# Optimization experiments

Hardware: AMD Instinct MI355X
Metric: run time of the kernel (lower is better)

The kernel has to match this reference:

```python
import jax, jax.numpy as jnp
import numpy as np

VOXEL_SIZE = 0.05  # init kwarg


def setup_inputs() -> dict:
    key = jax.random.key(0)
    N, B = 4_194_304, 16
    # coords uniform in [0, 5)^3 -> ~100^3 voxel cells per scene at voxel_size=0.05
    coord = jax.random.uniform(key, (N, 3), dtype=jnp.float32) * 5.0
    # cumulative batch offsets (equal-sized scenes), as pointops expects
    offset = (jnp.arange(1, B + 1, dtype=jnp.int32) * (N // B)).astype(jnp.int32)
    return {"coord": coord, "offset": offset}


def _voxel_mean(coord, offset, voxel_size):
    """Faithful jax port of voxelize_helper + segment_csr(mean) + batch2offset.

    Returns:
      n_p    [N,3]  voxel-mean coords, padded with zeros beyond n_voxels
      n_o    [B]    cumulative voxel counts per batch (batch2offset)
      counts [N]    points per voxel (idx_ptr = concat([0], cumsum(counts[valid])))
    """
    N = coord.shape[0]
    B = offset.shape[0]
    # batch id per point from cumulative offsets
    batch = jnp.searchsorted(offset, jnp.arange(N), side='right')  # [N]
    # start = per-batch min coord (start=None path of voxelize_helper)
    start = jax.ops.segment_min(coord, batch, num_segments=B)      # [B,3]
    grid = jnp.floor((coord - start[batch]) / voxel_size).astype(jnp.int32)  # [N,3]
    G = jnp.max(grid) + 1  # grid extent (per-axis upper bound)
    # linearized cluster key: unique per (batch, gx, gy, gz)
    ckey = ((batch * G + grid[:, 0]) * G + grid[:, 1]) * G + grid[:, 2]
    fill = B * G * G * G  # sentinel beyond any real key
    # sorted unique cluster keys == CSR segment order after sorting cluster indices
    uniq, inv = jnp.unique(ckey, return_inverse=True, size=N, fill_value=fill)
    # fused gather + segment-mean (equivalent to coord[sorted_idx] -> segment_csr mean)
    seg_sum = jax.ops.segment_sum(coord, inv, num_segments=N)                 # [N,3]
    counts = jax.ops.segment_sum(jnp.ones((N,), coord.dtype), inv, num_segments=N)
    n_p = seg_sum / jnp.maximum(counts, 1.0)[:, None]
    # batch id per voxel -> batch2offset (cumulative voxel counts)
    valid = uniq < fill
    vbatch = jnp.where(valid, uniq // (G * G * G), B)
    per_batch = jax.ops.segment_sum(valid.astype(jnp.int32), vbatch, num_segments=B + 1)[:B]
    n_o = jnp.cumsum(per_batch)
    return n_p, n_o, counts.astype(jnp.int32)


def reference(coord, offset):
    return _voxel_mean(coord, offset, VOXEL_SIZE)
```

## Files before the change

### kernel.cpp

```cpp
#include <hip/hip_runtime.h>
#include <stdint.h>


typedef unsigned int uint;
typedef unsigned long long u64;

#define VS 0.05f
#define QSCALE (4096.0f / VS)
#define QINV  (VS / 4096.0f)
#define NBUCKET 2048
#define CPB 16384
#define NBLK_P 256
#define DENSE_MAX 8192

__device__ __forceinline__ uint f2m(float f) {
    uint b = __float_as_uint(f);
    return (b & 0x80000000u) ? ~b : (b | 0x80000000u);
}
__device__ __forceinline__ float m2f(uint m) {
    uint b = (m & 0x80000000u) ? (m & 0x7fffffffu) : ~m;
    return __uint_as_float(b);
}

__global__ void k_init(uint* start_m, int B3) {
    int i = blockIdx.x * blockDim.x + threadIdx.x;
    if (i < B3) start_m[i] = 0xFFFFFFFFu;
}

__global__ void k_minmax(const float* __restrict__ coord, const int* __restrict__ offset,
                         int N, int B, uint* start_m) {
    __shared__ uint smin[768];
    __shared__ int soff[256];
    int nb3 = B * 3;
    for (int j = threadIdx.x; j < B; j += blockDim.x) soff[j] = offset[j];
    for (int j = threadIdx.x; j < nb3; j += blockDim.x) smin[j] = 0xFFFFFFFFu;
    __syncthreads();
    int lane = threadIdx.x & 63;
    int stride = gridDim.x * blockDim.x;
    for (int i = blockIdx.x * blockDim.x + threadIdx.x; i < N; i += stride) {
        float x = coord[3 * i + 0], y = coord[3 * i + 1], z = coord[3 * i + 2];
        int b = 0;
        for (int j = 0; j < B; ++j) b += (i >= soff[j]) ? 1 : 0;
        int wavebase = i - lane;
        bool full = (wavebase + 64 <= N);
        if (full && __all(b == __shfl(b, 0))) {
            float mnx = x, mny = y, mnz = z;
            for (int d = 32; d; d >>= 1) {
                mnx = fminf(mnx, __shfl_xor(mnx, d));
                mny = fminf(mny, __shfl_xor(mny, d));
                mnz = fminf(mnz, __shfl_xor(mnz, d));
            }
            if (lane == 0) {
                atomicMin(&smin[b * 3 + 0], f2m(mnx));
                atomicMin(&smin[b * 3 + 1], f2m(mny));
                atomicMin(&smin[b * 3 + 2], f2m(mnz));
            }
        } else {
            atomicMin(&smin[b * 3 + 0], f2m(x));
            atomicMin(&smin[b * 3 + 1], f2m(y));
            atomicMin(&smin[b * 3 + 2], f2m(z));
        }
    }
    __syncthreads();
    for (int j = threadIdx.x; j < nb3; j += blockDim.x) {
        uint mn = smin[j];
        if (mn != 0xFFFFFFFFu) atomicMin(&start_m[j], mn);
    }
}

__device__ __forceinline__ void point_grid(const float* __restrict__ coord, int i,
                                           const int* soff, const float* sstart, int B,
                                           float& x, float& y, float& z,
                                           int& b, int& gx, int& gy, int& gz) {
    x = coord[3 * i + 0]; y = coord[3 * i + 1]; z = coord[3 * i + 2];
    b = 0;
    for (int j = 0; j < B; ++j) b += (i >= soff[j]) ? 1 : 0;
    gx = min((int)floorf((x - sstart[b * 3 + 0]) / VS), 127);
    gy = min((int)floorf((y - sstart[b * 3 + 1]) / VS), 127);
    gz = min((int)floorf((z - sstart[b * 3 + 2]) / VS), 127);
}

__device__ __forceinline__ u64 frac12(float x, float y, float z,
                                      const float* sstart, int b,
                                      int gx, int gy, int gz) {
    float fx = fmaxf(x - (sstart[b * 3 + 0] + (float)gx * VS), 0.0f);
    float fy = fmaxf(y - (sstart[b * 3 + 1] + (float)gy * VS), 0.0f);
    float fz = fmaxf(z - (sstart[b * 3 + 2] + (float)gz * VS), 0.0f);
    uint ux = min((uint)(fx * QSCALE + 0.5f), 4095u);
    uint uy = min((uint)(fy * QSCALE + 0.5f), 4095u);
    uint uz = min((uint)(fz * QSCALE + 0.5f), 4095u);
    return ((u64)ux << 24) | ((u64)uy << 12) | (u64)uz;
}


__global__ void __launch_bounds__(1024)
k_count(const float* __restrict__ coord, const int* __restrict__ offset,
        int N, int B, const uint* __restrict__ start_m, uint* __restrict__ histm) {
    __shared__ uint hist[NBUCKET];
    __shared__ int soff[16];
    __shared__ float sstart[48];
    int t = threadIdx.x;
    if (t < B) soff[t] = offset[t];
    if (t < B * 3) sstart[t] = m2f(start_m[t]);
    for (int j = t; j < NBUCKET; j += blockDim.x) hist[j] = 0;
    __syncthreads();
    int chunk = (N + gridDim.x - 1) / gridDim.x;
    int lo = blockIdx.x * chunk, hi = min(N, lo + chunk);
    for (int i = lo + t; i < hi; i += blockDim.x) {
        float x, y, z; int b, gx, gy, gz;
        point_grid(coord, i, soff, sstart, B, x, y, z, b, gx, gy, gz);
        atomicAdd(&hist[(b << 7) | gx], 1u);
    }
    __syncthreads();
    for (int j = t; j < NBUCKET; j += blockDim.x)
        histm[(size_t)j * NBLK_P + blockIdx.x] = hist[j];
}

__global__ void k_scanrow(uint* __restrict__ histm, uint* __restrict__ tot) {
    __shared__ uint sc[256];
    uint* row = histm + (size_t)blockIdx.x * NBLK_P;
    int t = threadIdx.x;
    uint v = row[t];
    sc[t] = v;
    __syncthreads();
    for (int d = 1; d < 256; d <<= 1) {
        uint add = (t >= d) ? sc[t - d] : 0;
        __syncthreads();
        sc[t] += add;
        __syncthreads();
    }
    row[t] = sc[t] - v;
    if (t == 255) tot[blockIdx.x] = sc[255];
}

__global__ void k_scan2048(const uint* __restrict__ in, uint* __restrict__ out) {
    __shared__ uint p[1024];
    int t = threadIdx.x;
    uint a = in[2 * t], bb = in[2 * t + 1];
    p[t] = a + bb;
    __syncthreads();
    for (int d = 1; d < 1024; d <<= 1) {
        uint add = (t >= d) ? p[t - d] : 0;
        __syncthreads();
        p[t] += add;
        __syncthreads();
    }
    uint ex = p[t] - (a + bb);
    out[2 * t] = ex;
    out[2 * t + 1] = ex + a;
    if (t == 1023) out[2048] = p[1023];
}

__global__ void __launch_bounds__(1024)
k_partition(const float* __restrict__ coord, const int* __restrict__ offset,
            int N, int B, const uint* __restrict__ start_m,
            const uint* __restrict__ histm, const uint* __restrict__ bucket_base,
            u64* __restrict__ recs) {
    __shared__ uint cursor[NBUCKET];
    __shared__ int soff[16];
    __shared__ float sstart[48];
    int t = threadIdx.x;
    if (t < B) soff[t] = offset[t];
    if (t < B * 3) sstart[t] = m2f(start_m[t]);
    for (int j = t; j < NBUCKET; j += blockDim.x)
        cursor[j] = bucket_base[j] + histm[(size_t)j * NBLK_P + blockIdx.x];
    __syncthreads();
    int chunk = (N + gridDim.x - 1) / gridDim.x;
    int lo = blockIdx.x * chunk, hi = min(N, lo + chunk);
    for (int i = lo + t; i < hi; i += blockDim.x) {
        float x, y, z; int b, gx, gy, gz;
        point_grid(coord, i, soff, sstart, B, x, y, z, b, gx, gy, gz);
        uint cell = ((uint)gy << 7) | (uint)gz;
        u64 rec = ((u64)cell << 36) | frac12(x, y, z, sstart, b, gx, gy, gz);
        uint slot = atomicAdd(&cursor[(b << 7) | gx], 1u);
        recs[slot] = rec;
    }
}

__global__ void k_vox(const u64* __restrict__ recs, const uint* __restrict__ bucket_base,
                      uint* __restrict__ voxcount, uint* __restrict__ gmask) {
    __shared__ uint bits[512];
    __shared__ uint wsum[4];
    int q = blockIdx.x;
    uint lo = bucket_base[q], hi = bucket_base[q + 1];
    for (int j = threadIdx.x; j < 512; j += blockDim.x) bits[j] = 0;
    __syncthreads();
    for (uint i = lo + threadIdx.x; i < hi; i += blockDim.x) {
        uint c = (uint)(recs[i] >> 36);
        atomicOr(&bits[c >> 5], 1u << (c & 31));
    }
    __syncthreads();
    uint s = 0;
    for (int w = threadIdx.x; w < 512; w += blockDim.x) {
        uint m = bits[w];
        gmask[(size_t)q * 512 + w] = m;
        s += __popc(m);
    }
    for (int d = 32; d; d >>= 1) s += __shfl_xor(s, d);
    if ((threadIdx.x & 63) == 0) wsum[threadIdx.x >> 6] = s;
    __syncthreads();
    if (threadIdx.x == 0) voxcount[q] = wsum[0] + wsum[1] + wsum[2] + wsum[3];
}

__global__ void k_no3(const uint* __restrict__ voxscan, int B, float* __restrict__ no_out) {
    int t = threadIdx.x;
    if (t < B) no_out[t] = (float)voxscan[(t + 1) << 7];
}

__global__ void __launch_bounds__(1024)
k_emit2(const u64* __restrict__ recs, const uint* __restrict__ bucket_base,
        const uint* __restrict__ voxscan, const uint* __restrict__ gmask,
        const uint* __restrict__ start_m, float* __restrict__ np_out,
        float* __restrict__ cnt_out) {
    __shared__ u64 dense[DENSE_MAX];
    __shared__ uint mask[512], wrank[512];
    __shared__ uint svc;
    __shared__ float sstart[48];
    int q = blockIdx.x;
    uint lo = bucket_base[q], hi = bucket_base[q + 1];
    if (lo == hi) return;
    int t = threadIdx.x;
    if (t < 48) sstart[t] = m2f(start_m[t]);
    if (t < 512) {
        uint m = gmask[(size_t)q * 512 + t];
        mask[t] = m;
        wrank[t] = __popc(m);
    }
    __syncthreads();
    for (int d = 1; d < 512; d <<= 1) {
        uint add = (t < 512 && t >= d) ? wrank[t - d] : 0;
        __syncthreads();
        if (t < 512) wrank[t] += add;
        __syncthreads();
    }
    if (t == 511) svc = wrank[511];
    if (t < 512) wrank[t] -= __popc(mask[t]);
    __syncthreads();
    uint vc = svc;
    uint base_r = voxscan[q];
    int b = q >> 7, gx = q & 127;
    float cx = sstart[b * 3 + 0] + (float)gx * VS;
    float sy = sstart[b * 3 + 1], sz = sstart[b * 3 + 2];
    for (uint segbase = 0; segbase < vc; segbase += DENSE_MAX) {
        uint seglen = min(vc - segbase, (uint)DENSE_MAX);
        for (uint j = t; j < seglen; j += 1024) dense[j] = 0ull;
        __syncthreads();
        for (uint i = lo + t; i < hi; i += 1024) {
            u64 rec = recs[i];
            uint c = (uint)(rec >> 36);
            uint w = c >> 5, bit = c & 31;
            uint r = wrank[w] + __popc(mask[w] & ((1u << bit) - 1u));
            if (r >= segbase && r < segbase + seglen) {
                u64 enc = (((rec >> 24) & 0xFFFull) << 46) | (((rec >> 12) & 0xFFFull) << 28)
                        | ((rec & 0xFFFull) << 10) | 1ull;
                atomicAdd(&dense[r - segbase], enc);
            }
        }
        __syncthreads();
        for (uint rr = segbase + t; rr < segbase + seglen; rr += 1024) {
            uint l2 = 0, h2 = 511;
            while (l2 < h2) {
                uint mid = (l2 + h2 + 1) >> 1;
                if (wrank[mid] <= rr) l2 = mid; else h2 = mid - 1;
            }
            uint w = l2;
            uint idx = rr - wrank[w];
            uint m = mask[w], bit = 0, c;
            c = __popc(m & 0xFFFFu); if (idx >= c) { idx -= c; bit += 16; m >>= 16; }
            c = __popc(m & 0xFFu);   if (idx >= c) { idx -= c; bit += 8;  m >>= 8; }
            c = __popc(m & 0xFu);    if (idx >= c) { idx -= c; bit += 4;  m >>= 4; }
            c = __popc(m & 0x3u);    if (idx >= c) { idx -= c; bit += 2;  m >>= 2; }
            c = __popc(m & 0x1u);    if (idx >= c) { bit += 1; }
            uint cell = (w << 5) + bit;
            uint gy = cell >> 7, gz = cell & 127u;
            u64 p = dense[rr - segbase];
            float cnt = (float)(uint)(p & 1023ull);
            float inv = 1.0f / fmaxf(cnt, 1.0f);
            uint uz = (uint)((p >> 10) & 0x3FFFFull);
            uint uy = (uint)((p >> 28) & 0x3FFFFull);
            uint ux = (uint)(p >> 46);
            uint r_out = base_r + rr;
            np_out[3 * r_out + 0] = cx + ((float)ux * QINV) * inv;
            np_out[3 * r_out + 1] = sy + (float)gy * VS + ((float)uy * QINV) * inv;
            np_out[3 * r_out + 2] = sz + (float)gz * VS + ((float)uz * QINV) * inv;
            cnt_out[r_out] = cnt;
        }
        __syncthreads();
    }
}


__global__ void k_hist(const float* __restrict__ coord, const int* __restrict__ offset,
                       int N, int B, const uint* __restrict__ start_m,
                       uint* __restrict__ mask) {
    __shared__ int soff[256];
    __shared__ float sstart[768];
    for (int j = threadIdx.x; j < B; j += blockDim.x) soff[j] = offset[j];
    for (int j = threadIdx.x; j < B * 3; j += blockDim.x) sstart[j] = m2f(start_m[j]);
    __syncthreads();
    int i = blockIdx.x * blockDim.x + threadIdx.x;
    if (i >= N) return;
    float x, y, z; int b, gx, gy, gz;
    point_grid(coord, i, soff, sstart, B, x, y, z, b, gx, gy, gz);
    uint key = ((uint)b << 21) | ((uint)gx << 14) | ((uint)gy << 7) | (uint)gz;
    atomicOr(&mask[key >> 5], 1u << (key & 31));
}

__global__ void k_scan1(const uint* __restrict__ mask, uint* __restrict__ partial) {
    int base = blockIdx.x * 1024 + threadIdx.x * 4;
    uint4 m = *(const uint4*)(mask + base);
    uint s = __popc(m.x) + __popc(m.y) + __popc(m.z) + __popc(m.w);
    for (int d = 32; d; d >>= 1) s += __shfl_xor(s, d);
    __shared__ uint wsum[4];
    if ((threadIdx.x & 63) == 0) wsum[threadIdx.x >> 6] = s;
    __syncthreads();
    if (threadIdx.x == 0) partial[blockIdx.x] = wsum[0] + wsum[1] + wsum[2] + wsum[3];
}

__global__ void k_scan2(uint* partial, int P, uint* total) {
    __shared__ uint t[256];
    uint carry = 0;
    for (int base = 0; base < P; base += 256) {
        int j = base + threadIdx.x;
        uint v = (j < P) ? partial[j] : 0;
        t[threadIdx.x] = v;
        __syncthreads();
        for (int d = 1; d < 256; d <<= 1) {
            uint add = (threadIdx.x >= d) ? t[threadIdx.x - d] : 0;
            __syncthreads();
            t[threadIdx.x] += add;
            __syncthreads();
        }
        uint inc = t[threadIdx.x];
        uint chunk = t[255];
        if (j < P) partial[j] = carry + inc - v;
        __syncthreads();
        carry += chunk;
    }
    if (threadIdx.x == 0) *total = carry;
}

__global__ void k_scan3(const uint* __restrict__ mask, const uint* __restrict__ partial,
                        uint* __restrict__ wordrank) {
    int base = blockIdx.x * 1024 + threadIdx.x * 4;
    uint4 m = *(const uint4*)(mask + base);
    uint c0 = __popc(m.x), c1 = __popc(m.y), c2 = __popc(m.z), c3 = __popc(m.w);
    uint s = c0 + c1 + c2 + c3;
    __shared__ uint t[256];
    t[threadIdx.x] = s;
    __syncthreads();
    for (int d = 1; d < 256; d <<= 1) {
        uint add = (threadIdx.x >= d) ? t[threadIdx.x - d] : 0;
        __syncthreads();
        t[threadIdx.x] += add;
        __syncthreads();
    }
    uint ex = t[threadIdx.x] - s + partial[blockIdx.x];
    uint4 r;
    r.x = ex; r.y = ex + c0; r.z = ex + c0 + c1; r.w = ex + c0 + c1 + c2;
    *(uint4*)(wordrank + base) = r;
}

__global__ void k_no(const uint* mask, const uint* wordrank, const uint* total,
                     float* no_out, int B, int W) {
    int b = blockIdx.x * blockDim.x + threadIdx.x;
    if (b >= B) return;
    long long idx = (long long)(b + 1) << 21;
    uint w = (uint)(idx >> 5);
    uint v;
    if (w >= (uint)W) v = *total;
    else v = wordrank[w];
    no_out[b] = (float)v;
}

__global__ void k_accum_sparse(const float* __restrict__ coord, const int* __restrict__ offset,
                               int N, int B, const uint* __restrict__ start_m,
                               const uint* __restrict__ mask, const uint* __restrict__ wordrank,
                               u64* __restrict__ packed) {
    __shared__ int soff[256];
    __shared__ float sstart[768];
    for (int j = threadIdx.x; j < B; j += blockDim.x) soff[j] = offset[j];
    for (int j = threadIdx.x; j < B * 3; j += blockDim.x) sstart[j] = m2f(start_m[j]);
    __syncthreads();
    int i = blockIdx.x * blockDim.x + threadIdx.x;
    if (i >= N) return;
    float x, y, z; int b, gx, gy, gz;
    point_grid(coord, i, soff, sstart, B, x, y, z, b, gx, gy, gz);
    uint key = ((uint)b << 21) | ((uint)gx << 14) | ((uint)gy << 7) | (uint)gz;
    uint w = key >> 5, bit = key & 31;
    uint r = wordrank[w] + __popc(mask[w] & ((1u << bit) - 1u));
    u64 f = frac12(x, y, z, sstart, b, gx, gy, gz);
    u64 enc = (((f >> 24) & 0xFFFull) << 46) | (((f >> 12) & 0xFFFull) << 28)
            | ((f & 0xFFFull) << 10) | 1ull;
    atomicAdd(&packed[r], enc);
}

__global__ void k_decode_sparse(const uint* __restrict__ mask, const uint* __restrict__ wordrank,
                                const uint* __restrict__ start_m,
                                const u64* __restrict__ packed, int W,
                                float* __restrict__ np_out, float* __restrict__ cnt_out) {
    __shared__ float sstart[48];
    for (int j = threadIdx.x; j < 48; j += blockDim.x) sstart[j] = m2f(start_m[j]);
    __syncthreads();
    int w = blockIdx.x * blockDim.x + threadIdx.x;
    if (w >= W) return;
    uint m = mask[w];
    if (m == 0) return;
    uint r = wordrank[w];
    uint kbase = (uint)w << 5;
    while (m) {
        uint bit = (uint)__ffs(m) - 1u;
        m &= m - 1u;
        uint key = kbase + bit;
        u64 p = packed[r];
        float cnt = (float)(uint)(p & 1023ull);
        float inv = 1.0f / fmaxf(cnt, 1.0f);
        uint uz = (uint)((p >> 10) & 0x3FFFFull);
        uint uy = (uint)((p >> 28) & 0x3FFFFull);
        uint ux = (uint)(p >> 46);
        uint b = key >> 21;
        uint gx = (key >> 14) & 127u;
        uint gy = (key >> 7) & 127u;
        uint gz = key & 127u;
        np_out[3 * r + 0] = sstart[b * 3 + 0] + (float)gx * VS + ((float)ux * QINV) * inv;
        np_out[3 * r + 1] = sstart[b * 3 + 1] + (float)gy * VS + ((float)uy * QINV) * inv;
        np_out[3 * r + 2] = sstart[b * 3 + 2] + (float)gz * VS + ((float)uz * QINV) * inv;
        cnt_out[r] = cnt;
        ++r;
    }
}

extern "C" void kernel_launch(void* const* d_in, const int* in_sizes, int n_in,
                              void* d_out, int out_size, void* d_ws, size_t ws_size,
                              hipStream_t stream) {
    const float* coord = (const float*)d_in[0];
    const int* offset = (const int*)d_in[1];
    int N = in_sizes[0] / 3;
    int B = in_sizes[1];

    float* out = (float*)d_out;
    float* np_out = out;
    float* no_out = out + (size_t)3 * N;
    float* cnt_out = no_out + B;

    uint8_t* base = (uint8_t*)d_ws;
    uint* start_m = (uint*)base;
    uint* total = start_m + (size_t)B * 3;

    uintptr_t p = (uintptr_t)(total + 1);
    p = (p + 255) & ~(uintptr_t)255;
    uint* histm = (uint*)p;          p += (size_t)NBUCKET * NBLK_P * 4;
    p = (p + 255) & ~(uintptr_t)255;
    uint* tot = (uint*)p;            p += (size_t)NBUCKET * 4;
    p = (p + 255) & ~(uintptr_t)255;
    uint* bucket_base = (uint*)p;    p += (size_t)(NBUCKET + 1) * 4;
    p = (p + 255) & ~(uintptr_t)255;
    uint* voxcount = (uint*)p;       p += (size_t)NBUCKET * 4;
    p = (p + 255) & ~(uintptr_t)255;
    uint* voxscan = (uint*)p;        p += (size_t)(NBUCKET + 1) * 4;
    p = (p + 255) & ~(uintptr_t)255;
    uint* gmask = (uint*)p;          p += (size_t)NBUCKET * 512 * 4;
    p = (p + 255) & ~(uintptr_t)255;
    u64* recs = (u64*)p;             p += (size_t)N * 8;
    size_t need_part = p - (uintptr_t)base;

    hipMemsetAsync(d_out, 0, (size_t)out_size * sizeof(float), stream);
    k_init<<<(B * 3 + 255) / 256, 256, 0, stream>>>(start_m, B * 3);
    k_minmax<<<2048, 256, 0, stream>>>(coord, offset, N, B, start_m);

    if (B <= 16 && ws_size >= need_part) {
        k_count<<<NBLK_P, 1024, 0, stream>>>(coord, offset, N, B, start_m, histm);
        k_scanrow<<<NBUCKET, 256, 0, stream>>>(histm, tot);
        k_scan2048<<<1, 1024, 0, stream>>>(tot, bucket_base);
        k_partition<<<NBLK_P, 1024, 0, stream>>>(coord, offset, N, B, start_m, histm,
                                                 bucket_base, recs);
        k_vox<<<NBUCKET, 256, 0, stream>>>(recs, bucket_base, voxcount, gmask);
        k_scan2048<<<1, 1024, 0, stream>>>(voxcount, voxscan);
        k_no3<<<1, 64, 0, stream>>>(voxscan, B, no_out);
        k_emit2<<<NBUCKET, 1024, 0, stream>>>(recs, bucket_base, voxscan, gmask,
                                              start_m, np_out, cnt_out);
    } else {
        size_t W = (size_t)B << 16;
        int nblk1 = (int)(W / 1024);
        uintptr_t sp = (uintptr_t)(total + 1);
        sp = (sp + 255) & ~(uintptr_t)255;
        uint* partial = (uint*)sp;   sp += (size_t)nblk1 * 4;
        sp = (sp + 255) & ~(uintptr_t)255;
        uint* mask = (uint*)sp;      sp += W * 4;
        sp = (sp + 255) & ~(uintptr_t)255;
        uint* wordrank = (uint*)sp;  sp += W * 4;
        sp = (sp + 255) & ~(uintptr_t)255;
        u64* packed = (u64*)sp;
        int nb = (N + 255) / 256;
        hipMemsetAsync(mask, 0, W * sizeof(uint), stream);
        hipMemsetAsync(packed, 0, (size_t)N * sizeof(u64), stream);
        k_hist<<<nb, 256, 0, stream>>>(coord, offset, N, B, start_m, mask);
        k_scan1<<<nblk1, 256, 0, stream>>>(mask, partial);
        k_scan2<<<1, 256, 0, stream>>>(partial, nblk1, total);
        k_scan3<<<nblk1, 256, 0, stream>>>(mask, partial, wordrank);
        k_no<<<(B + 63) / 64, 64, 0, stream>>>(mask, wordrank, total, no_out, B, (int)W);
        k_accum_sparse<<<nb, 256, 0, stream>>>(coord, offset, N, B, start_m, mask,
                                               wordrank, packed);
        k_decode_sparse<<<(int)((W + 255) / 256), 256, 0, stream>>>(mask, wordrank, start_m,
                                                                    packed, (int)W,
                                                                    np_out, cnt_out);
    }
}
```

Before: 231.7 us.

## Vectorize min-reduction loads and replace full output memset with tail zeroing

The per-batch min kernel now reads coordinates as float4 over a contiguous chunk per block. When a chunk lies within one batch it keeps running per-axis minima, rotating which axis each lane tracks, and skips the per-point batch search and wave votes. The full output memset is dropped on the fast path and replaced by a kernel that zeroes only the padding beyond the voxel count, which removes a large redundant write. This relies on the emit kernel writing every valid voxel slot, and the fallback path still uses the memset.

```diff
diff --git a/kernel.cpp b/kernel.cpp
--- a/kernel.cpp
+++ b/kernel.cpp
@@ -27,42 +27,98 @@
     if (i < B3) start_m[i] = 0xFFFFFFFFu;
 }
 
-__global__ void k_minmax(const float* __restrict__ coord, const int* __restrict__ offset,
-                         int N, int B, uint* start_m) {
+__global__ void __launch_bounds__(256)
+k_minmax(const float* __restrict__ coord, const int* __restrict__ offset,
+         int N, int B, uint* start_m) {
     __shared__ uint smin[768];
     __shared__ int soff[256];
+    int t = threadIdx.x;
     int nb3 = B * 3;
-    for (int j = threadIdx.x; j < B; j += blockDim.x) soff[j] = offset[j];
-    for (int j = threadIdx.x; j < nb3; j += blockDim.x) smin[j] = 0xFFFFFFFFu;
-    __syncthreads();
-    int lane = threadIdx.x & 63;
-    int stride = gridDim.x * blockDim.x;
-    for (int i = blockIdx.x * blockDim.x + threadIdx.x; i < N; i += stride) {
-        float x = coord[3 * i + 0], y = coord[3 * i + 1], z = coord[3 * i + 2];
-        int b = 0;
-        for (int j = 0; j < B; ++j) b += (i >= soff[j]) ? 1 : 0;
-        int wavebase = i - lane;
-        bool full = (wavebase + 64 <= N);
-        if (full && __all(b == __shfl(b, 0))) {
-            float mnx = x, mny = y, mnz = z;
-            for (int d = 32; d; d >>= 1) {
-                mnx = fminf(mnx, __shfl_xor(mnx, d));
-                mny = fminf(mny, __shfl_xor(mny, d));
-                mnz = fminf(mnz, __shfl_xor(mnz, d));
+    for (int j = t; j < B; j += 256) soff[j] = offset[j];
+    for (int j = t; j < nb3; j += 256) smin[j] = 0xFFFFFFFFu;
+    __syncthreads();
+
+    int F = 3 * N;
+    int NQ = F >> 2;
+    int per = (NQ + gridDim.x - 1) / gridDim.x;
+    int qlo = blockIdx.x * per;
+    int qhi = min(NQ, qlo + per);
+    const float4* __restrict__ c4 = reinterpret_cast<const float4*>(coord);
+
+    bool fast = false;
+    int bU = 0;
+    if (qlo < qhi) {
+        int pF = (4 * qlo) / 3;
+        int pL = (4 * qhi - 1) / 3;
+        int bF = 0, bL = 0;
+        for (int j = 0; j < B; ++j) {
+            bF += (pF >= soff[j]) ? 1 : 0;
+            bL += (pL >= soff[j]) ? 1 : 0;
+        }
+        fast = (bF == bL);
+        bU = bF;
+    }
+
+    if (fast) {
+        int q = qlo + t;
+        int p0 = q % 3;
+        float s0 = INFINITY, s1 = INFINITY, s2 = INFINITY;
+        for (;;) {
+            if (q >= qhi) break;
+            float4 v = c4[q];
+            s0 = fminf(s0, fminf(v.x, v.w)); s1 = fminf(s1, v.y); s2 = fminf(s2, v.z);
+            q += 256;
+            if (q >= qhi) break;
+            v = c4[q];
+            s1 = fminf(s1, fminf(v.x, v.w)); s2 = fminf(s2, v.y); s0 = fminf(s0, v.z);
+            q += 256;
+            if (q >= qhi) break;
+            v = c4[q];
+            s2 = fminf(s2, fminf(v.x, v.w)); s0 = fminf(s0, v.y); s1 = fminf(s1, v.z);
+            q += 256;
+        }
+        float ax, ay, az;
+        if (p0 == 0)      { ax = s0; ay = s1; az = s2; }
+        else if (p0 == 1) { ax = s2; ay = s0; az = s1; }
+        else              { ax = s1; ay = s2; az = s0; }
+        for (int d = 32; d; d >>= 1) {
+            ax = fminf(ax, __shfl_xor(ax, d));
+            ay = fminf(ay, __shfl_xor(ay, d));
+            az = fminf(az, __shfl_xor(az, d));
+        }
+        if ((t & 63) == 0 && ax < INFINITY) {
+            atomicMin(&smin[bU * 3 + 0], f2m(ax));
+            atomicMin(&smin[bU * 3 + 1], f2m(ay));
+            atomicMin(&smin[bU * 3 + 2], f2m(az));
+        }
+    } else {
+        for (int q = qlo + t; q < qhi; q += 256) {
+            float4 v = c4[q];
+            int e = 4 * q;
+            float vals[4] = {v.x, v.y, v.z, v.w};
+#pragma unroll
+            for (int k = 0; k < 4; ++k) {
+                int ee = e + k;
+                int pt = ee / 3;
+                int axis = ee - 3 * pt;
+                int b = 0;
+                for (int j = 0; j < B; ++j) b += (pt >= soff[j]) ? 1 : 0;
+                atomicMin(&smin[b * 3 + axis], f2m(vals[k]));
             }
-            if (lane == 0) {
-                atomicMin(&smin[b * 3 + 0], f2m(mnx));
-                atomicMin(&smin[b * 3 + 1], f2m(mny));
-                atomicMin(&smin[b * 3 + 2], f2m(mnz));
-            }
-        } else {
-            atomicMin(&smin[b * 3 + 0], f2m(x));
-            atomicMin(&smin[b * 3 + 1], f2m(y));
-            atomicMin(&smin[b * 3 + 2], f2m(z));
-        }
-    }
-    __syncthreads();
-    for (int j = threadIdx.x; j < nb3; j += blockDim.x) {
+        }
+    }
+
+    if (blockIdx.x == 0) {
+        for (int ee = 4 * NQ + t; ee < F; ee += 256) {
+            int pt = ee / 3;
+            int axis = ee - 3 * pt;
+            int b = 0;
+            for (int j = 0; j < B; ++j) b += (pt >= soff[j]) ? 1 : 0;
+            atomicMin(&smin[b * 3 + axis], f2m(coord[ee]));
+        }
+    }
+    __syncthreads();
+    for (int j = t; j < nb3; j += 256) {
         uint mn = smin[j];
         if (mn != 0xFFFFFFFFu) atomicMin(&start_m[j], mn);
     }
@@ -205,6 +261,17 @@
 __global__ void k_no3(const uint* __restrict__ voxscan, int B, float* __restrict__ no_out) {
     int t = threadIdx.x;
     if (t < B) no_out[t] = (float)voxscan[(t + 1) << 7];
+}
+
+__global__ void k_tailzero(const uint* __restrict__ voxscan, int N, int B, int out_total,
+                           float* __restrict__ np_out, float* __restrict__ cnt_out,
+                           float* __restrict__ out) {
+    uint total = voxscan[NBUCKET];
+    int stride = gridDim.x * blockDim.x;
+    int tid = blockIdx.x * blockDim.x + threadIdx.x;
+    for (int j = 3 * (int)total + tid; j < 3 * N; j += stride) np_out[j] = 0.0f;
+    for (int j = (int)total + tid; j < N; j += stride) cnt_out[j] = 0.0f;
+    for (int j = 4 * N + B + tid; j < out_total; j += stride) out[j] = 0.0f;
 }
 
 __global__ void __launch_bounds__(1024)
@@ -464,7 +531,6 @@
     u64* recs = (u64*)p;             p += (size_t)N * 8;
     size_t need_part = p - (uintptr_t)base;
 
-    hipMemsetAsync(d_out, 0, (size_t)out_size * sizeof(float), stream);
     k_init<<<(B * 3 + 255) / 256, 256, 0, stream>>>(start_m, B * 3);
     k_minmax<<<2048, 256, 0, stream>>>(coord, offset, N, B, start_m);
 
@@ -477,9 +543,12 @@
         k_vox<<<NBUCKET, 256, 0, stream>>>(recs, bucket_base, voxcount, gmask);
         k_scan2048<<<1, 1024, 0, stream>>>(voxcount, voxscan);
         k_no3<<<1, 64, 0, stream>>>(voxscan, B, no_out);
+        k_tailzero<<<1024, 256, 0, stream>>>(voxscan, N, B, out_size,
+                                             np_out, cnt_out, out);
         k_emit2<<<NBUCKET, 1024, 0, stream>>>(recs, bucket_base, voxscan, gmask,
                                               start_m, np_out, cnt_out);
     } else {
+        hipMemsetAsync(d_out, 0, (size_t)out_size * sizeof(float), stream);
         size_t W = (size_t)B << 16;
         int nblk1 = (int)(W / 1024);
         uintptr_t sp = (uintptr_t)(total + 1);
```

Measured after the change: 206.6 us. -10.8%, faster.
